# Kernel optimization log

Hardware: AMD Instinct MI355X
Metric: run time of the kernel (lower is better)

## Reference

```python
import jax, jax.numpy as jnp
import numpy as np

N_NODES = 10000
N_EDGES = 160000
N_GRAPHS = 64
X_IN = 128
HID = 64
EDGE_DIM = 16
HEADS = 4
# (in_dim, out_dim_per_head) for the 3 TransformerConv layers (concat=False)
DIMS = [(X_IN, HID), (HID, 2 * HID), (2 * HID, HID)]
WNAMES = [f"{n}{l}" for l in (1, 2, 3) for n in ("wq", "bq", "wk", "bk", "wv", "bv", "we", "ws", "bs")]


def setup_inputs() -> dict:
    key = jax.random.key(0)
    ks = iter(jax.random.split(key, 64))
    inp = {}
    inp["x"] = jax.random.normal(next(ks), (N_NODES, X_IN), jnp.float32)
    inp["edge_index"] = jax.random.randint(next(ks), (2, N_EDGES), 0, N_NODES)
    inp["edge_attr"] = jax.random.normal(next(ks), (N_EDGES, EDGE_DIM), jnp.float32)
    inp["batch"] = jnp.sort(jax.random.randint(next(ks), (N_NODES,), 0, N_GRAPHS))
    for l, (din, dout) in enumerate(DIMS, 1):
        hd = HEADS * dout
        for nm, shape in [("wq", (din, hd)), ("wk", (din, hd)), ("wv", (din, hd)),
                          ("we", (EDGE_DIM, hd)), ("ws", (din, dout))]:
            inp[f"{nm}{l}"] = jax.random.normal(next(ks), shape, jnp.float32) * 0.05
        inp[f"bq{l}"] = jnp.zeros((hd,), jnp.float32)
        inp[f"bk{l}"] = jnp.zeros((hd,), jnp.float32)
        inp[f"bv{l}"] = jnp.zeros((hd,), jnp.float32)
        inp[f"bs{l}"] = jnp.zeros((dout,), jnp.float32)
    return inp


def _transformer_conv(x, src, dst, edge_attr, wq, bq, wk, bk, wv, bv, we, ws, bs, dout):
    """PyG TransformerConv, concat=False, root_weight=True, with edge features."""
    N = x.shape[0]
    q = (x @ wq + bq).reshape(N, HEADS, dout)
    k = (x @ wk + bk).reshape(N, HEADS, dout)
    v = (x @ wv + bv).reshape(N, HEADS, dout)
    e = (edge_attr @ we).reshape(-1, HEADS, dout)  # [E, H, C]
    k_j = k[src] + e                               # edge-conditioned keys
    alpha = jnp.einsum("ehd,ehd->eh", q[dst], k_j) * (1.0 / float(dout) ** 0.5)  # [E, H]
    # numerically stable segment softmax over incoming edges of each dst node
    a_max = jax.ops.segment_max(alpha, dst, num_segments=N)
    ex = jnp.exp(alpha - a_max[dst])
    den = jax.ops.segment_sum(ex, dst, num_segments=N)
    attn = ex / den[dst]
    agg = jax.ops.segment_sum((v[src] + e) * attn[..., None], dst, num_segments=N)  # [N, H, C]
    return agg.mean(axis=1) + x @ ws + bs  # concat=False -> head mean; + skip


def _forward(x, edge_attr, edge_index, batch, params):
    src, dst = edge_index[0], edge_index[1]
    h = x
    for l, (_, dout) in enumerate(DIMS, 1):
        p = [params[f"{n}{l}"] for n in ("wq", "bq", "wk", "bk", "wv", "bv", "we", "ws", "bs")]
        h = jax.nn.elu(_transformer_conv(h, src, dst, edge_attr, *p, dout))
    # global mean pool over graphs
    s = jax.ops.segment_sum(h, batch, num_segments=N_GRAPHS)
    cnt = jax.ops.segment_sum(jnp.ones((h.shape[0], 1), h.dtype), batch, num_segments=N_GRAPHS)
    return s / jnp.maximum(cnt, 1.0)


def reference(x, edge_index, edge_attr, batch,
              wq1, bq1, wk1, bk1, wv1, bv1, we1, ws1, bs1,
              wq2, bq2, wk2, bk2, wv2, bv2, we2, ws2, bs2,
              wq3, bq3, wk3, bk3, wv3, bv3, we3, ws3, bs3):
    params = dict(locals())
    return _forward(x, edge_attr, edge_index, batch, params)
```

## Files before the change

kernel.cpp:

```cpp
#include <hip/hip_runtime.h>
#include <hip/hip_fp16.h>
#include <math.h>

#define N_NODES 10000
#define N_EDGES 160000
#define N_GRAPHS 64

using half8 = __attribute__((ext_vector_type(8))) _Float16;
using floatx4 = __attribute__((ext_vector_type(4))) float;

template <int NV> struct KW;
template <> struct KW<1> { using T = uint2; };
template <> struct KW<2> { using T = uint4; };

__device__ inline void cvt_kv(const uint2& w, float4* dst) {
  float2 a = __half22float2(*reinterpret_cast<const __half2*>(&w.x));
  float2 b = __half22float2(*reinterpret_cast<const __half2*>(&w.y));
  dst[0] = make_float4(a.x, a.y, b.x, b.y);
}
__device__ inline void cvt_kv(const uint4& w, float4* dst) {
  float2 a = __half22float2(*reinterpret_cast<const __half2*>(&w.x));
  float2 b = __half22float2(*reinterpret_cast<const __half2*>(&w.y));
  float2 c = __half22float2(*reinterpret_cast<const __half2*>(&w.z));
  float2 d = __half22float2(*reinterpret_cast<const __half2*>(&w.w));
  dst[0] = make_float4(a.x, a.y, b.x, b.y);
  dst[1] = make_float4(c.x, c.y, d.x, d.y);
}

template <int K, int HD, int DOUT>
__global__ __launch_bounds__(256) void gemm_mfma(
    const __half* __restrict__ A, const __half* __restrict__ Wp,
    const float* __restrict__ bias, __half* __restrict__ QS,
    __half* __restrict__ KV, int M) {
  constexpr int QSS = HD + 64 + DOUT;
  constexpr int KVS = 2 * HD;
  constexpr int KS = K / 32;
  __shared__ __half st[64][72];
  const int tid = threadIdx.x;
  const int wave = tid >> 6, lane = tid & 63;
  const int quad = lane >> 4, n16 = lane & 15;
  const int row0 = blockIdx.y * 64;
  const int col0 = blockIdx.x * 64;
  const int nblk0 = blockIdx.x * 4;

  const int arow = min(row0 + wave * 16 + n16, M - 1);
  half8 afrag[KS];
#pragma unroll
  for (int s = 0; s < KS; ++s)
    afrag[s] = *reinterpret_cast<const half8*>(A + (size_t)arow * K + s * 32 + quad * 8);

  floatx4 acc[4];
#pragma unroll
  for (int t = 0; t < 4; ++t) {
    acc[t] = (floatx4){0.f, 0.f, 0.f, 0.f};
#pragma unroll
    for (int s = 0; s < KS; ++s) {
      half8 bf = *reinterpret_cast<const half8*>(
          Wp + (((size_t)(nblk0 + t) * KS + s) * 64 + lane) * 8);
      acc[t] = __builtin_amdgcn_mfma_f32_16x16x32_f16(afrag[s], bf, acc[t], 0, 0, 0);
    }
  }

#pragma unroll
  for (int t = 0; t < 4; ++t) {
    float bv = bias[col0 + t * 16 + n16];
#pragma unroll
    for (int r = 0; r < 4; ++r)
      st[wave * 16 + quad * 4 + r][t * 16 + n16] = __float2half(acc[t][r] + bv);
  }
  __syncthreads();

  __half* dp;
  int colb, stride;
  if (col0 < HD + 64) {
    dp = QS; colb = col0; stride = QSS;
  } else if (col0 < 3 * HD + 64) {
    dp = KV; colb = col0 - HD - 64; stride = KVS;
  } else {
    dp = QS; colb = HD + 64 + (col0 - 3 * HD - 64); stride = QSS;
  }
  for (int c = tid; c < 512; c += 256) {
    int r = c >> 3, seg = c & 7;
    int row = row0 + r;
    if (row < M)
      *reinterpret_cast<uint4*>(dp + (size_t)row * stride + colb + seg * 8) =
          *reinterpret_cast<const uint4*>(&st[r][seg * 8]);
  }
}

__device__ inline void pack_layer(int i, int K, int HD, int DOUT, float scale,
                                  const float* wq, const float* wk,
                                  const float* wv, const float* wsk,
                                  const float* we, const float* bq,
                                  const float* bk, const float* bv,
                                  const float* bs, __half* Wp, float* bcat) {
  const int W = 3 * HD + DOUT + 64;
  const int KS = K / 32;
  if (i < K * W) {
    int j = i & 7, lane = (i >> 3) & 63, fs = i >> 9;
    int nblk = fs / KS, s = fs - nblk * KS;
    int quad = lane >> 4, n = lane & 15;
    int k = s * 32 + quad * 8 + j, c = nblk * 16 + n;
    float v;
    if (c < HD) {
      v = wq[k * HD + c] * scale;
    } else if (c < HD + 64) {
      int gi = c - HD, hh = gi >> 4, d = gi & 15;
      float a = 0.f;
      for (int cc = 0; cc < DOUT; ++cc)
        a += wq[k * HD + hh * DOUT + cc] * we[d * HD + hh * DOUT + cc];
      v = a * scale;
    } else if (c < 2 * HD + 64) {
      v = wk[k * HD + (c - HD - 64)];
    } else if (c < 3 * HD + 64) {
      v = wv[k * HD + (c - 2 * HD - 64)];
    } else {
      v = wsk[k * DOUT + (c - 3 * HD - 64)];
    }
    Wp[i] = __float2half(v);
  } else {
    int c = i - K * W;
    float v;
    if (c < HD) {
      v = bq[c] * scale;
    } else if (c < HD + 64) {
      int gi = c - HD, hh = gi >> 4, d = gi & 15;
      float a = 0.f;
      for (int cc = 0; cc < DOUT; ++cc)
        a += bq[hh * DOUT + cc] * we[d * HD + hh * DOUT + cc];
      v = a * scale;
    } else if (c < 2 * HD + 64) {
      v = bk[c - HD - 64];
    } else if (c < 3 * HD + 64) {
      v = bv[c - 2 * HD - 64];
    } else {
      v = bs[c - 3 * HD - 64];
    }
    bcat[c] = v;
  }
}

#define T1 115584
#define T2 227904
#define T3 343488
#define TCONV (N_NODES * 32)
#define TTOT (T3 + TCONV)

__global__ void pack_all(
    const float* wq1, const float* wk1, const float* wv1, const float* ws1,
    const float* we1, const float* bq1, const float* bk1, const float* bv1,
    const float* bs1,
    const float* wq2, const float* wk2, const float* wv2, const float* ws2,
    const float* we2, const float* bq2, const float* bk2, const float* bv2,
    const float* bs2,
    const float* wq3, const float* wk3, const float* wv3, const float* ws3,
    const float* we3, const float* bq3, const float* bk3, const float* bv3,
    const float* bs3,
    __half* W1, float* b1, __half* W2, float* b2, __half* W3, float* b3,
    const float* x, __half* x16) {
  const float SC1 = 0.125f, SC2 = 0.08838834764831845f;
  for (int i = blockIdx.x * blockDim.x + threadIdx.x; i < TTOT;
       i += gridDim.x * blockDim.x) {
    if (i < T1)
      pack_layer(i, 128, 256, 64, SC1, wq1, wk1, wv1, ws1, we1, bq1, bk1, bv1, bs1, W1, b1);
    else if (i < T2)
      pack_layer(i - T1, 64, 512, 128, SC2, wq2, wk2, wv2, ws2, we2, bq2, bk2, bv2, bs2, W2, b2);
    else if (i < T3)
      pack_layer(i - T2, 128, 256, 64, SC1, wq3, wk3, wv3, ws3, we3, bq3, bk3, bv3, bs3, W3, b3);
    else {
      int k = i - T3;
      float4 v = reinterpret_cast<const float4*>(x)[k];
      __half2* o = reinterpret_cast<__half2*>(x16) + 2 * k;
      o[0] = __floats2half2_rn(v.x, v.y);
      o[1] = __floats2half2_rn(v.z, v.w);
    }
  }
}

__global__ void count_dst(const int* __restrict__ dst, int* __restrict__ cnt) {
  int e = blockIdx.x * blockDim.x + threadIdx.x;
  if (e < N_EDGES) atomicAdd(&cnt[dst[e]], 1);
}

__global__ __launch_bounds__(1024) void scan_offs(const int* __restrict__ cnt,
                                                  int* __restrict__ offs,
                                                  int* __restrict__ perm) {
  __shared__ int part[1024];
  __shared__ int hist[256], hstart[256], hcur[256];
  const int t = threadIdx.x;
  const int chunk = (N_NODES + 1023) / 1024;
  const int b = t * chunk;
  const int e = min(N_NODES, b + chunk);
  if (t < 256) { hist[t] = 0; hcur[t] = 0; }
  __syncthreads();
  int s = 0;
  for (int i = b; i < e; ++i) {
    int d = cnt[i];
    s += d;
    atomicAdd(&hist[min(d, 255)], 1);
  }
  part[t] = s;
  __syncthreads();
  for (int off = 1; off < 1024; off <<= 1) {
    int v = (t >= off) ? part[t - off] : 0;
    __syncthreads();
    part[t] += v;
    __syncthreads();
  }
  if (t == 0) {
    int acc = 0;
    for (int bk = 255; bk >= 0; --bk) { hstart[bk] = acc; acc += hist[bk]; }
    offs[N_NODES] = part[1023];
  }
  __syncthreads();
  int pre = (t == 0) ? 0 : part[t - 1];
  for (int i = b; i < e; ++i) {
    offs[i] = pre;
    int d = cnt[i];
    pre += d;
    int bkt = min(d, 255);
    int pos = hstart[bkt] + atomicAdd(&hcur[bkt], 1);
    perm[pos] = i;
  }
}

__global__ void scatter_csr(const int* __restrict__ src, const int* __restrict__ dst,
                            const float* __restrict__ edge_attr,
                            const int* __restrict__ offs, int* __restrict__ cursor,
                            int* __restrict__ csr_src, float* __restrict__ csr_ea) {
  int e = blockIdx.x * blockDim.x + threadIdx.x;
  if (e < N_EDGES) {
    int d = dst[e];
    int pos = offs[d] + atomicAdd(&cursor[d], 1);
    csr_src[pos] = src[e];
    float4* o4 = reinterpret_cast<float4*>(csr_ea + (size_t)pos * 16);
    const float4* s4 = reinterpret_cast<const float4*>(edge_attr + (size_t)e * 16);
    o4[0] = s4[0]; o4[1] = s4[1]; o4[2] = s4[2]; o4[3] = s4[3];
  }
}

template <int DOUT, bool W32>
__global__ __launch_bounds__(128) void edge_attn(
    const __half* __restrict__ QS, const __half* __restrict__ KV,
    const float* __restrict__ we, const int* __restrict__ csr_src,
    const float* __restrict__ csr_ea, const int* __restrict__ offs,
    const int* __restrict__ perm, float* __restrict__ out,
    __half* __restrict__ out16) {
  constexpr int HD = 4 * DOUT;
  constexpr int QSS = HD + 64 + DOUT;
  constexpr int KVS = 2 * HD;
  constexpr int NV = DOUT / 64;
  using KWT = typename KW<NV>::T;

  const int lane = threadIdx.x & 63;
  const int h = lane >> 4, t16 = lane & 15;
  const int n = perm[blockIdx.x * 2 + (threadIdx.x >> 6)];
  const int c0 = t16 * 4 * NV;

  const __half* base = QS + (size_t)n * QSS;
  float4 q[NV], acc[NV];
  {
    KWT qw = *reinterpret_cast<const KWT*>(base + h * DOUT + c0);
    cvt_kv(qw, q);
  }
#pragma unroll
  for (int v = 0; v < NV; ++v) acc[v] = make_float4(0.f, 0.f, 0.f, 0.f);
  const float g = __half2float(base[HD + h * 16 + t16]);

  float lsum = 0.f, tacc = 0.f;

  const int s0 = offs[n], s1 = offs[n + 1];

  float eaA[4], eaB[4], eaC[4];
  KWT krA[4], vrA[4], krB[4], vrB[4], krC[4], vrC[4];

  for (int cb = s0; cb < s1; cb += 64) {
    const int m = min(64, s1 - cb);
    const int idx = csr_src[cb + min(lane, m - 1)];
    const int ng = m >> 2;

    auto load_grp = [&](int gb, float (&ea)[4], KWT (&kr)[4], KWT (&vr)[4]) {
      const int bi = cb + gb;
#pragma unroll
      for (int j = 0; j < 4; ++j) ea[j] = csr_ea[(size_t)(bi + j) * 16 + t16];
#pragma unroll
      for (int j = 0; j < 4; ++j) {
        int sj = __shfl(idx, gb + j);
        const __half* rb = KV + (size_t)sj * KVS + h * DOUT + c0;
        kr[j] = *reinterpret_cast<const KWT*>(rb);
        vr[j] = *reinterpret_cast<const KWT*>(rb + HD);
      }
    };

    auto compute_grp = [&](float (&ea)[4], KWT (&kr)[4], KWT (&vr)[4]) {
      float a[4];
#pragma unroll
      for (int j = 0; j < 4; ++j) {
        float4 kk[NV];
        cvt_kv(kr[j], kk);
        float p = ea[j] * g;
#pragma unroll
        for (int v = 0; v < NV; ++v)
          p += q[v].x * kk[v].x + q[v].y * kk[v].y + q[v].z * kk[v].z +
               q[v].w * kk[v].w;
        a[j] = p;
      }
#pragma unroll
      for (int j = 0; j < 4; ++j) {
        a[j] += __shfl_xor(a[j], 1);
        a[j] += __shfl_xor(a[j], 2);
        a[j] += __shfl_xor(a[j], 4);
        a[j] += __shfl_xor(a[j], 8);
      }
      float p0 = __expf(a[0]), p1 = __expf(a[1]);
      float p2 = __expf(a[2]), p3 = __expf(a[3]);
      lsum += p0 + p1 + p2 + p3;
      tacc += p0 * ea[0] + p1 * ea[1] + p2 * ea[2] + p3 * ea[3];
      float pj[4] = {p0, p1, p2, p3};
#pragma unroll
      for (int j = 0; j < 4; ++j) {
        float4 vv[NV];
        cvt_kv(vr[j], vv);
#pragma unroll
        for (int v = 0; v < NV; ++v) {
          acc[v].x += pj[j] * vv[v].x;
          acc[v].y += pj[j] * vv[v].y;
          acc[v].z += pj[j] * vv[v].z;
          acc[v].w += pj[j] * vv[v].w;
        }
      }
    };

    if (ng) {
      load_grp(0, eaA, krA, vrA);
      if (ng > 1) load_grp(4, eaB, krB, vrB);
      int gi = 0;
      for (;;) {
        if (gi + 2 < ng) load_grp((gi + 2) * 4, eaC, krC, vrC);
        compute_grp(eaA, krA, vrA);
        if (++gi >= ng) break;
        if (gi + 2 < ng) load_grp((gi + 2) * 4, eaA, krA, vrA);
        compute_grp(eaB, krB, vrB);
        if (++gi >= ng) break;
        if (gi + 2 < ng) load_grp((gi + 2) * 4, eaB, krB, vrB);
        compute_grp(eaC, krC, vrC);
        if (++gi >= ng) break;
      }
    }

    for (int e = ng * 4; e < m; ++e) {
      int sj = __shfl(idx, e);
      float ea0 = csr_ea[(size_t)(cb + e) * 16 + t16];
      const __half* rb = KV + (size_t)sj * KVS + h * DOUT + c0;
      KWT kw = *reinterpret_cast<const KWT*>(rb);
      KWT vw = *reinterpret_cast<const KWT*>(rb + HD);
      float4 kk[NV], vv[NV];
      cvt_kv(kw, kk);
      cvt_kv(vw, vv);
      float a = ea0 * g;
#pragma unroll
      for (int v = 0; v < NV; ++v)
        a += q[v].x * kk[v].x + q[v].y * kk[v].y + q[v].z * kk[v].z + q[v].w * kk[v].w;
      a += __shfl_xor(a, 1);
      a += __shfl_xor(a, 2);
      a += __shfl_xor(a, 4);
      a += __shfl_xor(a, 8);
      float p = __expf(a);
      lsum += p;
      tacc += p * ea0;
#pragma unroll
      for (int v = 0; v < NV; ++v) {
        acc[v].x += p * vv[v].x;
        acc[v].y += p * vv[v].y;
        acc[v].z += p * vv[v].z;
        acc[v].w += p * vv[v].w;
      }
    }
  }

  float invl = (lsum > 0.f) ? 1.f / lsum : 0.f;
  float tn = tacc * invl;
  float4 val[NV];
#pragma unroll
  for (int v = 0; v < NV; ++v) {
    val[v].x = acc[v].x * invl; val[v].y = acc[v].y * invl;
    val[v].z = acc[v].z * invl; val[v].w = acc[v].w * invl;
  }
#pragma unroll
  for (int d = 0; d < 16; ++d) {
    float td = __shfl(tn, (lane & 48) | d);
    const float* wb = we + d * HD + h * DOUT + c0;
#pragma unroll
    for (int v = 0; v < NV; ++v) {
      float4 w4 = *reinterpret_cast<const float4*>(wb + 4 * v);
      val[v].x += td * w4.x; val[v].y += td * w4.y;
      val[v].z += td * w4.z; val[v].w += td * w4.w;
    }
  }
#pragma unroll
  for (int v = 0; v < NV; ++v) {
    val[v].x += __shfl_xor(val[v].x, 16); val[v].x += __shfl_xor(val[v].x, 32);
    val[v].y += __shfl_xor(val[v].y, 16); val[v].y += __shfl_xor(val[v].y, 32);
    val[v].z += __shfl_xor(val[v].z, 16); val[v].z += __shfl_xor(val[v].z, 32);
    val[v].w += __shfl_xor(val[v].w, 16); val[v].w += __shfl_xor(val[v].w, 32);
  }
  if (h == 0) {
    KWT sw = *reinterpret_cast<const KWT*>(base + HD + 64 + c0);
    float4 sk[NV];
    cvt_kv(sw, sk);
#pragma unroll
    for (int v = 0; v < NV; ++v) {
      float4 o;
      o.x = 0.25f * val[v].x + sk[v].x;
      o.y = 0.25f * val[v].y + sk[v].y;
      o.z = 0.25f * val[v].z + sk[v].z;
      o.w = 0.25f * val[v].w + sk[v].w;
      o.x = (o.x > 0.f) ? o.x : expm1f(o.x);
      o.y = (o.y > 0.f) ? o.y : expm1f(o.y);
      o.z = (o.z > 0.f) ? o.z : expm1f(o.z);
      o.w = (o.w > 0.f) ? o.w : expm1f(o.w);
      if (W32)
        *reinterpret_cast<float4*>(out + (size_t)n * DOUT + c0 + 4 * v) = o;
      __half2* o16 = reinterpret_cast<__half2*>(out16 + (size_t)n * DOUT + c0 + 4 * v);
      o16[0] = __floats2half2_rn(o.x, o.y);
      o16[1] = __floats2half2_rn(o.z, o.w);
    }
  }
}

__device__ inline int lower_bound(const int* b, int n, int v) {
  int lo = 0, hi = n;
  while (lo < hi) {
    int mid = (lo + hi) >> 1;
    if (b[mid] < v) lo = mid + 1; else hi = mid;
  }
  return lo;
}

__global__ __launch_bounds__(256) void pool_all(const float* __restrict__ h,
                                                const int* __restrict__ batch,
                                                float* __restrict__ out) {
  const int g = blockIdx.x;
  const int start = lower_bound(batch, N_NODES, g);
  const int end = lower_bound(batch, N_NODES, g + 1);
  const int c = threadIdx.x & 63, j = threadIdx.x >> 6;
  float s = 0.f;
  for (int n = start + j; n < end; n += 4) s += h[(size_t)n * 64 + c];
  __shared__ float red[4][64];
  red[j][c] = s;
  __syncthreads();
  if (j == 0) {
    float tot = red[0][c] + red[1][c] + red[2][c] + red[3][c];
    out[g * 64 + c] = tot / (float)max(end - start, 1);
  }
}

extern "C" void kernel_launch(void* const* d_in, const int* in_sizes, int n_in,
                              void* d_out, int out_size, void* d_ws, size_t ws_size,
                              hipStream_t stream) {
  const float* x = (const float*)d_in[0];
  const int* edge_index = (const int*)d_in[1];
  const float* edge_attr = (const float*)d_in[2];
  const int* batch = (const int*)d_in[3];
  const int* srcp = edge_index;
  const int* dstp = edge_index + N_EDGES;

  const bool dict_order = in_sizes[5] > 1024;
  const float *wq[3], *wk[3], *wv[3], *wep[3], *wsk[3], *bq[3], *bk[3], *bv[3], *bs[3];
  for (int L = 0; L < 3; ++L) {
    int b = 4 + L * 9;
    if (dict_order) {
      wq[L] = (const float*)d_in[b + 0];
      wk[L] = (const float*)d_in[b + 1];
      wv[L] = (const float*)d_in[b + 2];
      wep[L] = (const float*)d_in[b + 3];
      wsk[L] = (const float*)d_in[b + 4];
      bq[L] = (const float*)d_in[b + 5];
      bk[L] = (const float*)d_in[b + 6];
      bv[L] = (const float*)d_in[b + 7];
      bs[L] = (const float*)d_in[b + 8];
    } else {
      wq[L] = (const float*)d_in[b + 0];
      bq[L] = (const float*)d_in[b + 1];
      wk[L] = (const float*)d_in[b + 2];
      bk[L] = (const float*)d_in[b + 3];
      wv[L] = (const float*)d_in[b + 4];
      bv[L] = (const float*)d_in[b + 5];
      wep[L] = (const float*)d_in[b + 6];
      wsk[L] = (const float*)d_in[b + 7];
      bs[L] = (const float*)d_in[b + 8];
    }
  }

  char* p = (char*)d_ws;
  __half* qs = (__half*)p;    p += (size_t)N_NODES * 704 * 2;
  __half* kv = (__half*)p;    p += (size_t)N_NODES * 1024 * 2;
  float* h1 = (float*)p;      p += (size_t)N_NODES * 64 * 4;
  __half* x16 = (__half*)p;   p += (size_t)N_NODES * 128 * 2;
  __half* h16 = (__half*)p;   p += (size_t)N_NODES * 128 * 2;
  __half* W1 = (__half*)p;    p += 128 * 896 * 2;
  __half* W2 = (__half*)p;    p += 64 * 1728 * 2;
  __half* W3 = (__half*)p;    p += 128 * 896 * 2;
  float* b1 = (float*)p;      p += 896 * 4;
  float* b2 = (float*)p;      p += 1728 * 4;
  float* b3 = (float*)p;      p += 896 * 4;
  float* csr_ea = (float*)p;  p += (size_t)N_EDGES * 16 * 4;
  int* cnt = (int*)p;         p += N_NODES * 4;
  int* cursor = (int*)p;      p += N_NODES * 4;
  int* offs = (int*)p;        p += (N_NODES + 1) * 4;
  int* perm = (int*)p;        p += N_NODES * 4;
  int* csr_src = (int*)p;     p += N_EDGES * 4;

  pack_all<<<1024, 256, 0, stream>>>(
      wq[0], wk[0], wv[0], wsk[0], wep[0], bq[0], bk[0], bv[0], bs[0],
      wq[1], wk[1], wv[1], wsk[1], wep[1], bq[1], bk[1], bv[1], bs[1],
      wq[2], wk[2], wv[2], wsk[2], wep[2], bq[2], bk[2], bv[2], bs[2],
      W1, b1, W2, b2, W3, b3, x, x16);

  hipMemsetAsync(cnt, 0, 2 * N_NODES * sizeof(int), stream);
  count_dst<<<(N_EDGES + 255) / 256, 256, 0, stream>>>(dstp, cnt);
  scan_offs<<<1, 1024, 0, stream>>>(cnt, offs, perm);
  scatter_csr<<<(N_EDGES + 255) / 256, 256, 0, stream>>>(srcp, dstp, edge_attr,
                                                         offs, cursor, csr_src, csr_ea);

  const int MT = (N_NODES + 63) / 64;
  gemm_mfma<128, 256, 64><<<dim3(896 / 64, MT), 256, 0, stream>>>(x16, W1, b1, qs,
                                                                  kv, N_NODES);
  edge_attn<64, false><<<N_NODES / 2, 128, 0, stream>>>(qs, kv, wep[0], csr_src,
                                                        csr_ea, offs, perm, h1, h16);
  gemm_mfma<64, 512, 128><<<dim3(1728 / 64, MT), 256, 0, stream>>>(h16, W2, b2, qs,
                                                                   kv, N_NODES);
  edge_attn<128, false><<<N_NODES / 2, 128, 0, stream>>>(qs, kv, wep[1], csr_src,
                                                         csr_ea, offs, perm, h1, h16);
  gemm_mfma<128, 256, 64><<<dim3(896 / 64, MT), 256, 0, stream>>>(h16, W3, b3, qs,
                                                                  kv, N_NODES);
  edge_attn<64, true><<<N_NODES / 2, 128, 0, stream>>>(qs, kv, wep[2], csr_src,
                                                       csr_ea, offs, perm, h1, x16);

  pool_all<<<N_GRAPHS, 256, 0, stream>>>(h1, batch, (float*)d_out);
}
```

Before: 324.7 us.

## Process two nodes per wave with cross-node prefetch and fdot2 QK dot

Each wave now handles two destination nodes in sequence instead of one, and the grid is halved. The first edge group of the second node is loaded before the first node's epilogue runs, so those gathers overlap the epilogue work. The Q·K dot product now uses packed fp16 fdot2 instructions instead of converting both operands to fp32. This trades wave-level parallelism for latency hiding, and the fp16 dot changes rounding slightly.

```diff
diff --git a/kernel.cpp b/kernel.cpp
--- a/kernel.cpp
+++ b/kernel.cpp
@@ -8,6 +8,7 @@
 
 using half8 = __attribute__((ext_vector_type(8))) _Float16;
 using floatx4 = __attribute__((ext_vector_type(4))) float;
+using h2v = __attribute__((ext_vector_type(2))) _Float16;
 
 template <int NV> struct KW;
 template <> struct KW<1> { using T = uint2; };
@@ -26,6 +27,34 @@
   dst[0] = make_float4(a.x, a.y, b.x, b.y);
   dst[1] = make_float4(c.x, c.y, d.x, d.y);
 }
+
+#if __has_builtin(__builtin_amdgcn_fdot2)
+__device__ inline float dot_qk(const uint2& k, const uint2& q, float c) {
+  c = __builtin_amdgcn_fdot2(__builtin_bit_cast(h2v, k.x), __builtin_bit_cast(h2v, q.x), c, false);
+  c = __builtin_amdgcn_fdot2(__builtin_bit_cast(h2v, k.y), __builtin_bit_cast(h2v, q.y), c, false);
+  return c;
+}
+__device__ inline float dot_qk(const uint4& k, const uint4& q, float c) {
+  c = __builtin_amdgcn_fdot2(__builtin_bit_cast(h2v, k.x), __builtin_bit_cast(h2v, q.x), c, false);
+  c = __builtin_amdgcn_fdot2(__builtin_bit_cast(h2v, k.y), __builtin_bit_cast(h2v, q.y), c, false);
+  c = __builtin_amdgcn_fdot2(__builtin_bit_cast(h2v, k.z), __builtin_bit_cast(h2v, q.z), c, false);
+  c = __builtin_amdgcn_fdot2(__builtin_bit_cast(h2v, k.w), __builtin_bit_cast(h2v, q.w), c, false);
+  return c;
+}
+#else
+__device__ inline float dot_qk(const uint2& k, const uint2& q, float c) {
+  float4 kk[1], qq[1];
+  cvt_kv(k, kk); cvt_kv(q, qq);
+  return c + qq[0].x * kk[0].x + qq[0].y * kk[0].y + qq[0].z * kk[0].z + qq[0].w * kk[0].w;
+}
+__device__ inline float dot_qk(const uint4& k, const uint4& q, float c) {
+  float4 kk[2], qq[2];
+  cvt_kv(k, kk); cvt_kv(q, qq);
+  c += qq[0].x * kk[0].x + qq[0].y * kk[0].y + qq[0].z * kk[0].z + qq[0].w * kk[0].w;
+  c += qq[1].x * kk[1].x + qq[1].y * kk[1].y + qq[1].z * kk[1].z + qq[1].w * kk[1].w;
+  return c;
+}
+#endif
 
 template <int K, int HD, int DOUT>
 __global__ __launch_bounds__(256) void gemm_mfma(
@@ -254,178 +283,196 @@
 
   const int lane = threadIdx.x & 63;
   const int h = lane >> 4, t16 = lane & 15;
-  const int n = perm[blockIdx.x * 2 + (threadIdx.x >> 6)];
   const int c0 = t16 * 4 * NV;
-
-  const __half* base = QS + (size_t)n * QSS;
-  float4 q[NV], acc[NV];
-  {
-    KWT qw = *reinterpret_cast<const KWT*>(base + h * DOUT + c0);
-    cvt_kv(qw, q);
-  }
-#pragma unroll
-  for (int v = 0; v < NV; ++v) acc[v] = make_float4(0.f, 0.f, 0.f, 0.f);
-  const float g = __half2float(base[HD + h * 16 + t16]);
-
-  float lsum = 0.f, tacc = 0.f;
-
-  const int s0 = offs[n], s1 = offs[n + 1];
-
-  float eaA[4], eaB[4], eaC[4];
-  KWT krA[4], vrA[4], krB[4], vrB[4], krC[4], vrC[4];
-
-  for (int cb = s0; cb < s1; cb += 64) {
-    const int m = min(64, s1 - cb);
-    const int idx = csr_src[cb + min(lane, m - 1)];
-    const int ng = m >> 2;
-
-    auto load_grp = [&](int gb, float (&ea)[4], KWT (&kr)[4], KWT (&vr)[4]) {
-      const int bi = cb + gb;
-#pragma unroll
-      for (int j = 0; j < 4; ++j) ea[j] = csr_ea[(size_t)(bi + j) * 16 + t16];
-#pragma unroll
-      for (int j = 0; j < 4; ++j) {
-        int sj = __shfl(idx, gb + j);
-        const __half* rb = KV + (size_t)sj * KVS + h * DOUT + c0;
-        kr[j] = *reinterpret_cast<const KWT*>(rb);
-        vr[j] = *reinterpret_cast<const KWT*>(rb + HD);
-      }
-    };
-
-    auto compute_grp = [&](float (&ea)[4], KWT (&kr)[4], KWT (&vr)[4]) {
-      float a[4];
-#pragma unroll
-      for (int j = 0; j < 4; ++j) {
-        float4 kk[NV];
-        cvt_kv(kr[j], kk);
-        float p = ea[j] * g;
-#pragma unroll
-        for (int v = 0; v < NV; ++v)
-          p += q[v].x * kk[v].x + q[v].y * kk[v].y + q[v].z * kk[v].z +
-               q[v].w * kk[v].w;
-        a[j] = p;
-      }
-#pragma unroll
-      for (int j = 0; j < 4; ++j) {
-        a[j] += __shfl_xor(a[j], 1);
-        a[j] += __shfl_xor(a[j], 2);
-        a[j] += __shfl_xor(a[j], 4);
-        a[j] += __shfl_xor(a[j], 8);
-      }
-      float p0 = __expf(a[0]), p1 = __expf(a[1]);
-      float p2 = __expf(a[2]), p3 = __expf(a[3]);
-      lsum += p0 + p1 + p2 + p3;
-      tacc += p0 * ea[0] + p1 * ea[1] + p2 * ea[2] + p3 * ea[3];
-      float pj[4] = {p0, p1, p2, p3};
-#pragma unroll
-      for (int j = 0; j < 4; ++j) {
-        float4 vv[NV];
-        cvt_kv(vr[j], vv);
-#pragma unroll
-        for (int v = 0; v < NV; ++v) {
-          acc[v].x += pj[j] * vv[v].x;
-          acc[v].y += pj[j] * vv[v].y;
-          acc[v].z += pj[j] * vv[v].z;
-          acc[v].w += pj[j] * vv[v].w;
+  const int pbase = (blockIdx.x * 2 + (threadIdx.x >> 6)) * 2;
+  const int nA = perm[pbase], nB = perm[pbase + 1];
+  const __half* baseA = QS + (size_t)nA * QSS;
+  const __half* baseB = QS + (size_t)nB * QSS;
+
+  const int s0A = offs[nA], s1A = offs[nA + 1];
+  const int s0B = offs[nB], s1B = offs[nB + 1];
+  KWT qwA = *reinterpret_cast<const KWT*>(baseA + h * DOUT + c0);
+  KWT qwB = *reinterpret_cast<const KWT*>(baseB + h * DOUT + c0);
+  const float gA = __half2float(baseA[HD + h * 16 + t16]);
+  const float gB = __half2float(baseB[HD + h * 16 + t16]);
+  int idxA = (s1A > s0A) ? csr_src[s0A + min(lane, s1A - s0A - 1)] : 0;
+  int idxB = (s1B > s0B) ? csr_src[s0B + min(lane, s1B - s0B - 1)] : 0;
+
+  float ea0[4], ea1[4], ea2[4];
+  KWT kr0[4], vr0[4], kr1[4], vr1[4], kr2[4], vr2[4];
+  float4 acc[NV];
+  float lsum, tacc;
+
+  auto run_node = [&](int s0, int s1, int idx0, float g, KWT qw, bool pre0) {
+    lsum = 0.f; tacc = 0.f;
+#pragma unroll
+    for (int v = 0; v < NV; ++v) acc[v] = make_float4(0.f, 0.f, 0.f, 0.f);
+    int idx = idx0;
+    for (int cb = s0; cb < s1; cb += 64) {
+      const int m = min(64, s1 - cb);
+      if (cb != s0) idx = csr_src[cb + min(lane, m - 1)];
+      const int ng = m >> 2;
+
+      auto load_grp = [&](int gb, float (&ea)[4], KWT (&kr)[4], KWT (&vr)[4]) {
+        const int bi = cb + gb;
+#pragma unroll
+        for (int j = 0; j < 4; ++j) ea[j] = csr_ea[(size_t)(bi + j) * 16 + t16];
+#pragma unroll
+        for (int j = 0; j < 4; ++j) {
+          int sj = __shfl(idx, gb + j);
+          const __half* rb = KV + (size_t)sj * KVS + h * DOUT + c0;
+          kr[j] = *reinterpret_cast<const KWT*>(rb);
+          vr[j] = *reinterpret_cast<const KWT*>(rb + HD);
+        }
+      };
+
+      auto compute_grp = [&](float (&ea)[4], KWT (&kr)[4], KWT (&vr)[4]) {
+        float a[4];
+#pragma unroll
+        for (int j = 0; j < 4; ++j) a[j] = dot_qk(kr[j], qw, ea[j] * g);
+#pragma unroll
+        for (int j = 0; j < 4; ++j) {
+          a[j] += __shfl_xor(a[j], 1);
+          a[j] += __shfl_xor(a[j], 2);
+          a[j] += __shfl_xor(a[j], 4);
+          a[j] += __shfl_xor(a[j], 8);
+        }
+        float p0 = __expf(a[0]), p1 = __expf(a[1]);
+        float p2 = __expf(a[2]), p3 = __expf(a[3]);
+        lsum += p0 + p1 + p2 + p3;
+        tacc += p0 * ea[0] + p1 * ea[1] + p2 * ea[2] + p3 * ea[3];
+        float pj[4] = {p0, p1, p2, p3};
+#pragma unroll
+        for (int j = 0; j < 4; ++j) {
+          float4 vv[NV];
+          cvt_kv(vr[j], vv);
+#pragma unroll
+          for (int v = 0; v < NV; ++v) {
+            acc[v].x += pj[j] * vv[v].x;
+            acc[v].y += pj[j] * vv[v].y;
+            acc[v].z += pj[j] * vv[v].z;
+            acc[v].w += pj[j] * vv[v].w;
+          }
+        }
+      };
+
+      if (ng) {
+        if (!(cb == s0 && pre0)) load_grp(0, ea0, kr0, vr0);
+        if (ng > 1) load_grp(4, ea1, kr1, vr1);
+        int gi = 0;
+        for (;;) {
+          if (gi + 2 < ng) load_grp((gi + 2) * 4, ea2, kr2, vr2);
+          compute_grp(ea0, kr0, vr0);
+          if (++gi >= ng) break;
+          if (gi + 2 < ng) load_grp((gi + 2) * 4, ea0, kr0, vr0);
+          compute_grp(ea1, kr1, vr1);
+          if (++gi >= ng) break;
+          if (gi + 2 < ng) load_grp((gi + 2) * 4, ea1, kr1, vr1);
+          compute_grp(ea2, kr2, vr2);
+          if (++gi >= ng) break;
         }
       }
-    };
-
-    if (ng) {
-      load_grp(0, eaA, krA, vrA);
-      if (ng > 1) load_grp(4, eaB, krB, vrB);
-      int gi = 0;
-      for (;;) {
-        if (gi + 2 < ng) load_grp((gi + 2) * 4, eaC, krC, vrC);
-        compute_grp(eaA, krA, vrA);
-        if (++gi >= ng) break;
-        if (gi + 2 < ng) load_grp((gi + 2) * 4, eaA, krA, vrA);
-        compute_grp(eaB, krB, vrB);
-        if (++gi >= ng) break;
-        if (gi + 2 < ng) load_grp((gi + 2) * 4, eaB, krB, vrB);
-        compute_grp(eaC, krC, vrC);
-        if (++gi >= ng) break;
+
+      for (int e = ng * 4; e < m; ++e) {
+        int sj = __shfl(idx, e);
+        float ea0s = csr_ea[(size_t)(cb + e) * 16 + t16];
+        const __half* rb = KV + (size_t)sj * KVS + h * DOUT + c0;
+        KWT kw = *reinterpret_cast<const KWT*>(rb);
+        KWT vw = *reinterpret_cast<const KWT*>(rb + HD);
+        float a = dot_qk(kw, qw, ea0s * g);
+        a += __shfl_xor(a, 1);
+        a += __shfl_xor(a, 2);
+        a += __shfl_xor(a, 4);
+        a += __shfl_xor(a, 8);
+        float p = __expf(a);
+        lsum += p;
+        tacc += p * ea0s;
+        float4 vv[NV];
+        cvt_kv(vw, vv);
+#pragma unroll
+        for (int v = 0; v < NV; ++v) {
+          acc[v].x += p * vv[v].x;
+          acc[v].y += p * vv[v].y;
+          acc[v].z += p * vv[v].z;
+          acc[v].w += p * vv[v].w;
+        }
       }
     }
-
-    for (int e = ng * 4; e < m; ++e) {
-      int sj = __shfl(idx, e);
-      float ea0 = csr_ea[(size_t)(cb + e) * 16 + t16];
-      const __half* rb = KV + (size_t)sj * KVS + h * DOUT + c0;
-      KWT kw = *reinterpret_cast<const KWT*>(rb);
-      KWT vw = *reinterpret_cast<const KWT*>(rb + HD);
-      float4 kk[NV], vv[NV];
-      cvt_kv(kw, kk);
-      cvt_kv(vw, vv);
-      float a = ea0 * g;
-#pragma unroll
-      for (int v = 0; v < NV; ++v)
-        a += q[v].x * kk[v].x + q[v].y * kk[v].y + q[v].z * kk[v].z + q[v].w * kk[v].w;
-      a += __shfl_xor(a, 1);
-      a += __shfl_xor(a, 2);
-      a += __shfl_xor(a, 4);
-      a += __shfl_xor(a, 8);
-      float p = __expf(a);
-      lsum += p;
-      tacc += p * ea0;
+  };
+
+  auto epi = [&](int n, const __half* base) {
+    float invl = (lsum > 0.f) ? 1.f / lsum : 0.f;
+    float tn = tacc * invl;
+    float4 val[NV];
+#pragma unroll
+    for (int v = 0; v < NV; ++v) {
+      val[v].x = acc[v].x * invl; val[v].y = acc[v].y * invl;
+      val[v].z = acc[v].z * invl; val[v].w = acc[v].w * invl;
+    }
+#pragma unroll
+    for (int d = 0; d < 16; ++d) {
+      float td = __shfl(tn, (lane & 48) | d);
+      const float* wb = we + d * HD + h * DOUT + c0;
 #pragma unroll
       for (int v = 0; v < NV; ++v) {
-        acc[v].x += p * vv[v].x;
-        acc[v].y += p * vv[v].y;
-        acc[v].z += p * vv[v].z;
-        acc[v].w += p * vv[v].w;
+        float4 w4 = *reinterpret_cast<const float4*>(wb + 4 * v);
+        val[v].x += td * w4.x; val[v].y += td * w4.y;
+        val[v].z += td * w4.z; val[v].w += td * w4.w;
       }
     }
-  }
-
-  float invl = (lsum > 0.f) ? 1.f / lsum : 0.f;
-  float tn = tacc * invl;
-  float4 val[NV];
-#pragma unroll
-  for (int v = 0; v < NV; ++v) {
-    val[v].x = acc[v].x * invl; val[v].y = acc[v].y * invl;
-    val[v].z = acc[v].z * invl; val[v].w = acc[v].w * invl;
-  }
-#pragma unroll
-  for (int d = 0; d < 16; ++d) {
-    float td = __shfl(tn, (lane & 48) | d);
-    const float* wb = we + d * HD + h * DOUT + c0;
 #pragma unroll
     for (int v = 0; v < NV; ++v) {
-      float4 w4 = *reinterpret_cast<const float4*>(wb + 4 * v);
-      val[v].x += td * w4.x; val[v].y += td * w4.y;
-      val[v].z += td * w4.z; val[v].w += td * w4.w;
-    }
-  }
-#pragma unroll
-  for (int v = 0; v < NV; ++v) {
-    val[v].x += __shfl_xor(val[v].x, 16); val[v].x += __shfl_xor(val[v].x, 32);
-    val[v].y += __shfl_xor(val[v].y, 16); val[v].y += __shfl_xor(val[v].y, 32);
-    val[v].z += __shfl_xor(val[v].z, 16); val[v].z += __shfl_xor(val[v].z, 32);
-    val[v].w += __shfl_xor(val[v].w, 16); val[v].w += __shfl_xor(val[v].w, 32);
-  }
-  if (h == 0) {
-    KWT sw = *reinterpret_cast<const KWT*>(base + HD + 64 + c0);
-    float4 sk[NV];
-    cvt_kv(sw, sk);
-#pragma unroll
-    for (int v = 0; v < NV; ++v) {
-      float4 o;
-      o.x = 0.25f * val[v].x + sk[v].x;
-      o.y = 0.25f * val[v].y + sk[v].y;
-      o.z = 0.25f * val[v].z + sk[v].z;
-      o.w = 0.25f * val[v].w + sk[v].w;
-      o.x = (o.x > 0.f) ? o.x : expm1f(o.x);
-      o.y = (o.y > 0.f) ? o.y : expm1f(o.y);
-      o.z = (o.z > 0.f) ? o.z : expm1f(o.z);
-      o.w = (o.w > 0.f) ? o.w : expm1f(o.w);
-      if (W32)
-        *reinterpret_cast<float4*>(out + (size_t)n * DOUT + c0 + 4 * v) = o;
-      __half2* o16 = reinterpret_cast<__half2*>(out16 + (size_t)n * DOUT + c0 + 4 * v);
-      o16[0] = __floats2half2_rn(o.x, o.y);
-      o16[1] = __floats2half2_rn(o.z, o.w);
-    }
-  }
+      val[v].x += __shfl_xor(val[v].x, 16); val[v].x += __shfl_xor(val[v].x, 32);
+      val[v].y += __shfl_xor(val[v].y, 16); val[v].y += __shfl_xor(val[v].y, 32);
+      val[v].z += __shfl_xor(val[v].z, 16); val[v].z += __shfl_xor(val[v].z, 32);
+      val[v].w += __shfl_xor(val[v].w, 16); val[v].w += __shfl_xor(val[v].w, 32);
+    }
+    if (h == 0) {
+      KWT sw = *reinterpret_cast<const KWT*>(base + HD + 64 + c0);
+      float4 sk[NV];
+      cvt_kv(sw, sk);
+#pragma unroll
+      for (int v = 0; v < NV; ++v) {
+        float4 o;
+        o.x = 0.25f * val[v].x + sk[v].x;
+        o.y = 0.25f * val[v].y + sk[v].y;
+        o.z = 0.25f * val[v].z + sk[v].z;
+        o.w = 0.25f * val[v].w + sk[v].w;
+        o.x = (o.x > 0.f) ? o.x : expm1f(o.x);
+        o.y = (o.y > 0.f) ? o.y : expm1f(o.y);
+        o.z = (o.z > 0.f) ? o.z : expm1f(o.z);
+        o.w = (o.w > 0.f) ? o.w : expm1f(o.w);
+        if (W32)
+          *reinterpret_cast<float4*>(out + (size_t)n * DOUT + c0 + 4 * v) = o;
+        __half2* o16 = reinterpret_cast<__half2*>(out16 + (size_t)n * DOUT + c0 + 4 * v);
+        o16[0] = __floats2half2_rn(o.x, o.y);
+        o16[1] = __floats2half2_rn(o.z, o.w);
+      }
+    }
+  };
+
+  run_node(s0A, s1A, idxA, gA, qwA, false);
+
+  bool preB = false;
+  {
+    const int mB = min(64, s1B - s0B);
+    if (mB >= 4) {
+#pragma unroll
+      for (int j = 0; j < 4; ++j) ea0[j] = csr_ea[(size_t)(s0B + j) * 16 + t16];
+#pragma unroll
+      for (int j = 0; j < 4; ++j) {
+        int sj = __shfl(idxB, j);
+        const __half* rb = KV + (size_t)sj * KVS + h * DOUT + c0;
+        kr0[j] = *reinterpret_cast<const KWT*>(rb);
+        vr0[j] = *reinterpret_cast<const KWT*>(rb + HD);
+      }
+      preB = true;
+    }
+  }
+  epi(nA, baseA);
+
+  run_node(s0B, s1B, idxB, gB, qwB, preB);
+  epi(nB, baseB);
 }
 
 __device__ inline int lower_bound(const int* b, int n, int v) {
@@ -526,15 +573,15 @@
   const int MT = (N_NODES + 63) / 64;
   gemm_mfma<128, 256, 64><<<dim3(896 / 64, MT), 256, 0, stream>>>(x16, W1, b1, qs,
                                                                   kv, N_NODES);
-  edge_attn<64, false><<<N_NODES / 2, 128, 0, stream>>>(qs, kv, wep[0], csr_src,
+  edge_attn<64, false><<<N_NODES / 4, 128, 0, stream>>>(qs, kv, wep[0], csr_src,
                                                         csr_ea, offs, perm, h1, h16);
   gemm_mfma<64, 512, 128><<<dim3(1728 / 64, MT), 256, 0, stream>>>(h16, W2, b2, qs,
                                                                    kv, N_NODES);
-  edge_attn<128, false><<<N_NODES / 2, 128, 0, stream>>>(qs, kv, wep[1], csr_src,
+  edge_attn<128, false><<<N_NODES / 4, 128, 0, stream>>>(qs, kv, wep[1], csr_src,
                                                          csr_ea, offs, perm, h1, h16);
   gemm_mfma<128, 256, 64><<<dim3(896 / 64, MT), 256, 0, stream>>>(h16, W3, b3, qs,
                                                                   kv, N_NODES);
-  edge_attn<64, true><<<N_NODES / 2, 128, 0, stream>>>(qs, kv, wep[2], csr_src,
+  edge_attn<64, true><<<N_NODES / 4, 128, 0, stream>>>(qs, kv, wep[2], csr_src,
                                                        csr_ea, offs, perm, h1, x16);
 
   pool_all<<<N_GRAPHS, 256, 0, stream>>>(h1, batch, (float*)d_out);
```

Result: slower. 350.3 us (+7.9%).

## Interleave K/V rows for single-load gathers and use packed fp16 dot2

Applied to the files above, without the earlier changes.

For layers where the per-head width is 64, the GEMM epilogue now writes K and V interleaved in 4-element chunks per head. Each edge-attention lane can then fetch its key and value with a single 16-byte gather instead of two 8-byte gathers. The query-key dot product now uses the packed fp16 fdot2 instruction on raw half data, which removes the per-element half-to-float conversions and separate FMAs. This reduces scattered memory transactions and ALU work in the edge-dominated kernel. It ties the KV layout to the epilogue and consumer staying in sync, and products are formed in fp16 precision inside fdot2.

```diff
diff --git a/kernel.cpp b/kernel.cpp
--- a/kernel.cpp
+++ b/kernel.cpp
@@ -8,6 +8,7 @@
 
 using half8 = __attribute__((ext_vector_type(8))) _Float16;
 using floatx4 = __attribute__((ext_vector_type(4))) float;
+using h2v = __attribute__((ext_vector_type(2))) _Float16;
 
 template <int NV> struct KW;
 template <> struct KW<1> { using T = uint2; };
@@ -26,6 +27,34 @@
   dst[0] = make_float4(a.x, a.y, b.x, b.y);
   dst[1] = make_float4(c.x, c.y, d.x, d.y);
 }
+
+#if __has_builtin(__builtin_amdgcn_fdot2)
+__device__ inline float dot_qk(const uint2& k, const uint2& q, float c) {
+  c = __builtin_amdgcn_fdot2(__builtin_bit_cast(h2v, k.x), __builtin_bit_cast(h2v, q.x), c, false);
+  c = __builtin_amdgcn_fdot2(__builtin_bit_cast(h2v, k.y), __builtin_bit_cast(h2v, q.y), c, false);
+  return c;
+}
+__device__ inline float dot_qk(const uint4& k, const uint4& q, float c) {
+  c = __builtin_amdgcn_fdot2(__builtin_bit_cast(h2v, k.x), __builtin_bit_cast(h2v, q.x), c, false);
+  c = __builtin_amdgcn_fdot2(__builtin_bit_cast(h2v, k.y), __builtin_bit_cast(h2v, q.y), c, false);
+  c = __builtin_amdgcn_fdot2(__builtin_bit_cast(h2v, k.z), __builtin_bit_cast(h2v, q.z), c, false);
+  c = __builtin_amdgcn_fdot2(__builtin_bit_cast(h2v, k.w), __builtin_bit_cast(h2v, q.w), c, false);
+  return c;
+}
+#else
+__device__ inline float dot_qk(const uint2& k, const uint2& q, float c) {
+  float4 kk[1], qq[1];
+  cvt_kv(k, kk); cvt_kv(q, qq);
+  return c + qq[0].x * kk[0].x + qq[0].y * kk[0].y + qq[0].z * kk[0].z + qq[0].w * kk[0].w;
+}
+__device__ inline float dot_qk(const uint4& k, const uint4& q, float c) {
+  float4 kk[2], qq[2];
+  cvt_kv(k, kk); cvt_kv(q, qq);
+  c += qq[0].x * kk[0].x + qq[0].y * kk[0].y + qq[0].z * kk[0].z + qq[0].w * kk[0].w;
+  c += qq[1].x * kk[1].x + qq[1].y * kk[1].y + qq[1].z * kk[1].z + qq[1].w * kk[1].w;
+  return c;
+}
+#endif
 
 template <int K, int HD, int DOUT>
 __global__ __launch_bounds__(256) void gemm_mfma(
@@ -35,6 +64,7 @@
   constexpr int QSS = HD + 64 + DOUT;
   constexpr int KVS = 2 * HD;
   constexpr int KS = K / 32;
+  constexpr int NV = DOUT / 64;
   __shared__ __half st[64][72];
   const int tid = threadIdx.x;
   const int wave = tid >> 6, lane = tid & 63;
@@ -72,19 +102,31 @@
 
   __half* dp;
   int colb, stride;
+  bool kvreg = false;
   if (col0 < HD + 64) {
     dp = QS; colb = col0; stride = QSS;
   } else if (col0 < 3 * HD + 64) {
-    dp = KV; colb = col0 - HD - 64; stride = KVS;
+    dp = KV; colb = col0 - HD - 64; stride = KVS; kvreg = true;
   } else {
     dp = QS; colb = HD + 64 + (col0 - 3 * HD - 64); stride = QSS;
   }
   for (int c = tid; c < 512; c += 256) {
     int r = c >> 3, seg = c & 7;
     int row = row0 + r;
-    if (row < M)
+    if (row >= M) continue;
+    if (NV == 1 && kvreg) {
+      int dfull = colb + seg * 8;
+      bool isK = dfull < HD;
+      int dd = isK ? dfull : dfull - HD;
+      int hh = dd >> 6, d0 = dd & 63;
+      int o = hh * 128 + 2 * d0 + (isK ? 0 : 4);
+      uint4 w = *reinterpret_cast<const uint4*>(&st[r][seg * 8]);
+      *reinterpret_cast<uint2*>(dp + (size_t)row * stride + o) = make_uint2(w.x, w.y);
+      *reinterpret_cast<uint2*>(dp + (size_t)row * stride + o + 8) = make_uint2(w.z, w.w);
+    } else {
       *reinterpret_cast<uint4*>(dp + (size_t)row * stride + colb + seg * 8) =
           *reinterpret_cast<const uint4*>(&st[r][seg * 8]);
+    }
   }
 }
 
@@ -256,13 +298,11 @@
   const int h = lane >> 4, t16 = lane & 15;
   const int n = perm[blockIdx.x * 2 + (threadIdx.x >> 6)];
   const int c0 = t16 * 4 * NV;
+  const int kvoff = h * 128 + t16 * 8;
 
   const __half* base = QS + (size_t)n * QSS;
-  float4 q[NV], acc[NV];
-  {
-    KWT qw = *reinterpret_cast<const KWT*>(base + h * DOUT + c0);
-    cvt_kv(qw, q);
-  }
+  KWT qw = *reinterpret_cast<const KWT*>(base + h * DOUT + c0);
+  float4 acc[NV];
 #pragma unroll
   for (int v = 0; v < NV; ++v) acc[v] = make_float4(0.f, 0.f, 0.f, 0.f);
   const float g = __half2float(base[HD + h * 16 + t16]);
@@ -272,38 +312,36 @@
   const int s0 = offs[n], s1 = offs[n + 1];
 
   float eaA[4], eaB[4], eaC[4];
-  KWT krA[4], vrA[4], krB[4], vrB[4], krC[4], vrC[4];
+  uint4 krA[4], vrA[4], krB[4], vrB[4], krC[4], vrC[4];
 
   for (int cb = s0; cb < s1; cb += 64) {
     const int m = min(64, s1 - cb);
     const int idx = csr_src[cb + min(lane, m - 1)];
     const int ng = m >> 2;
 
-    auto load_grp = [&](int gb, float (&ea)[4], KWT (&kr)[4], KWT (&vr)[4]) {
+    auto load_grp = [&](int gb, float (&ea)[4], uint4 (&kr)[4], uint4 (&vr)[4]) {
       const int bi = cb + gb;
 #pragma unroll
       for (int j = 0; j < 4; ++j) ea[j] = csr_ea[(size_t)(bi + j) * 16 + t16];
 #pragma unroll
       for (int j = 0; j < 4; ++j) {
         int sj = __shfl(idx, gb + j);
-        const __half* rb = KV + (size_t)sj * KVS + h * DOUT + c0;
-        kr[j] = *reinterpret_cast<const KWT*>(rb);
-        vr[j] = *reinterpret_cast<const KWT*>(rb + HD);
+        const __half* rb = KV + (size_t)sj * KVS + kvoff;
+        kr[j] = *reinterpret_cast<const uint4*>(rb);
+        if (NV == 2) vr[j] = *reinterpret_cast<const uint4*>(rb + HD);
       }
     };
 
-    auto compute_grp = [&](float (&ea)[4], KWT (&kr)[4], KWT (&vr)[4]) {
+    auto compute_grp = [&](float (&ea)[4], uint4 (&kr)[4], uint4 (&vr)[4]) {
       float a[4];
 #pragma unroll
       for (int j = 0; j < 4; ++j) {
-        float4 kk[NV];
-        cvt_kv(kr[j], kk);
-        float p = ea[j] * g;
-#pragma unroll
-        for (int v = 0; v < NV; ++v)
-          p += q[v].x * kk[v].x + q[v].y * kk[v].y + q[v].z * kk[v].z +
-               q[v].w * kk[v].w;
-        a[j] = p;
+        if (NV == 1)
+          a[j] = dot_qk(make_uint2(kr[j].x, kr[j].y),
+                        *reinterpret_cast<const uint2*>(&qw), ea[j] * g);
+        else
+          a[j] = dot_qk(*reinterpret_cast<const uint4*>(&kr[j]),
+                        *reinterpret_cast<const uint4*>(&qw), ea[j] * g);
       }
 #pragma unroll
       for (int j = 0; j < 4; ++j) {
@@ -320,7 +358,10 @@
 #pragma unroll
       for (int j = 0; j < 4; ++j) {
         float4 vv[NV];
-        cvt_kv(vr[j], vv);
+        if (NV == 1)
+          cvt_kv(make_uint2(kr[j].z, kr[j].w), vv);
+        else
+          cvt_kv(vr[j], vv);
 #pragma unroll
         for (int v = 0; v < NV; ++v) {
           acc[v].x += pj[j] * vv[v].x;
@@ -351,16 +392,19 @@
     for (int e = ng * 4; e < m; ++e) {
       int sj = __shfl(idx, e);
       float ea0 = csr_ea[(size_t)(cb + e) * 16 + t16];
-      const __half* rb = KV + (size_t)sj * KVS + h * DOUT + c0;
-      KWT kw = *reinterpret_cast<const KWT*>(rb);
-      KWT vw = *reinterpret_cast<const KWT*>(rb + HD);
-      float4 kk[NV], vv[NV];
-      cvt_kv(kw, kk);
-      cvt_kv(vw, vv);
-      float a = ea0 * g;
-#pragma unroll
-      for (int v = 0; v < NV; ++v)
-        a += q[v].x * kk[v].x + q[v].y * kk[v].y + q[v].z * kk[v].z + q[v].w * kk[v].w;
+      const __half* rb = KV + (size_t)sj * KVS + kvoff;
+      uint4 kw = *reinterpret_cast<const uint4*>(rb);
+      float a;
+      float4 vv[NV];
+      if (NV == 1) {
+        a = dot_qk(make_uint2(kw.x, kw.y),
+                   *reinterpret_cast<const uint2*>(&qw), ea0 * g);
+        cvt_kv(make_uint2(kw.z, kw.w), vv);
+      } else {
+        uint4 vw = *reinterpret_cast<const uint4*>(rb + HD);
+        a = dot_qk(kw, *reinterpret_cast<const uint4*>(&qw), ea0 * g);
+        cvt_kv(vw, vv);
+      }
       a += __shfl_xor(a, 1);
       a += __shfl_xor(a, 2);
       a += __shfl_xor(a, 4);
```

Measured after the change: 329.0 us. About the same (+1.3%).
